# Performance work log

Hardware: AMD Instinct MI355X
Metric: run time of the kernel (lower is better)

Reference implementation:

```python
import jax, jax.numpy as jnp
import numpy as np

N, E, D, H = 100000, 1600000, 128, 2
D2 = D * H  # conv2 output dim = out_dim * heads = 256


def setup_inputs() -> dict:
    key = jax.random.key(0)
    ks = jax.random.split(key, 9)
    x = jax.random.normal(ks[0], (N, D), dtype=jnp.float32)
    edge_index = jax.random.randint(ks[1], (2, E), 0, N, dtype=jnp.int64)
    edge_weight = jax.random.uniform(ks[2], (E,), dtype=jnp.float32)
    s = 1.0 / np.sqrt(D)
    W_rel1 = jax.random.normal(ks[3], (D, D), dtype=jnp.float32) * s
    W_root1 = jax.random.normal(ks[4], (D, D), dtype=jnp.float32) * s
    b1 = jnp.zeros((D,), dtype=jnp.float32)
    W_rel2 = jax.random.normal(ks[5], (D, D2), dtype=jnp.float32) * s
    W_root2 = jax.random.normal(ks[6], (D, D2), dtype=jnp.float32) * s
    b2 = jnp.zeros((D2,), dtype=jnp.float32)
    return {"x": x, "edge_index": edge_index, "edge_weight": edge_weight,
            "W_rel1": W_rel1, "b1": b1, "W_root1": W_root1,
            "W_rel2": W_rel2, "b2": b2, "W_root2": W_root2}


def _graph_conv(x, src, dst, edge_weight, W_rel, b, W_root, n_nodes):
    # message: w_e * x_src ; aggregate: mean over incoming edges at dst
    msgs = x[src] * edge_weight[:, None]                       # [E, D]
    summed = jax.ops.segment_sum(msgs, dst, num_segments=n_nodes)  # [N, D]
    cnt = jax.ops.segment_sum(jnp.ones((src.shape[0],), x.dtype), dst,
                              num_segments=n_nodes)
    mean = summed / jnp.maximum(cnt, 1.0)[:, None]
    # GraphConv: lin_rel(aggr) + lin_root(x); bias only on lin_rel
    return mean @ W_rel + b + x @ W_root


def reference(x, edge_index, edge_weight, W_rel1, b1, W_root1, W_rel2, b2, W_root2):
    src, dst = edge_index[0], edge_index[1]
    n = x.shape[0]
    h = _graph_conv(x, src, dst, edge_weight, W_rel1, b1, W_root1, n)
    out = _graph_conv(h, src, dst, edge_weight, W_rel2, b2, W_root2, n)
    return out
```

## Files before the change

### kernel.cpp

```cpp
#include <hip/hip_runtime.h>
#include <hip/hip_bf16.h>

#define D_IN 128
#define SORT_CHUNK 4096
#define NBUCK 256

typedef __attribute__((ext_vector_type(8))) short bf16x8;
typedef __attribute__((ext_vector_type(8))) unsigned short u16x8;
typedef __attribute__((ext_vector_type(4))) float f32x4;


__global__ __launch_bounds__(256) void scan_block_sums(const int* __restrict__ in,
                                                       int* __restrict__ partial,
                                                       int M) {
    __shared__ int sdata[256];
    int b = blockIdx.x, t = threadIdx.x;
    int base = b * 1024 + t * 4;
    int s = 0;
#pragma unroll
    for (int i = 0; i < 4; ++i) {
        int idx = base + i;
        if (idx < M) s += in[idx];
    }
    sdata[t] = s;
    __syncthreads();
    for (int off = 128; off > 0; off >>= 1) {
        if (t < off) sdata[t] += sdata[t + off];
        __syncthreads();
    }
    if (t == 0) partial[b] = sdata[0];
}

__global__ void scan_partials(int* __restrict__ partial, int nb) {
    if (threadIdx.x == 0 && blockIdx.x == 0) {
        int run = 0;
        for (int i = 0; i < nb; ++i) {
            int t = partial[i];
            partial[i] = run;
            run += t;
        }
    }
}

__global__ __launch_bounds__(256) void scan_final(const int* __restrict__ in,
                                                  const int* __restrict__ partial,
                                                  int* __restrict__ outS,
                                                  int M) {
    __shared__ int sdata[256];
    int b = blockIdx.x, t = threadIdx.x;
    int base = b * 1024 + t * 4;
    int v[4];
    int s = 0;
#pragma unroll
    for (int i = 0; i < 4; ++i) {
        int idx = base + i;
        v[i] = (idx < M) ? in[idx] : 0;
        s += v[i];
    }
    sdata[t] = s;
    __syncthreads();
    for (int o = 1; o < 256; o <<= 1) {
        int tmp = 0;
        if (t >= o) tmp = sdata[t - o];
        __syncthreads();
        sdata[t] += tmp;
        __syncthreads();
    }
    int run = partial[b] + (sdata[t] - s);
#pragma unroll
    for (int i = 0; i < 4; ++i) {
        int idx = base + i;
        if (idx < M) outS[idx] = run;
        run += v[i];
    }
}


__global__ __launch_bounds__(256) void bucket_hist_kernel(const int* __restrict__ dst,
                                                          int* __restrict__ bh,
                                                          long long E, int N, int nbe) {
    __shared__ int cnt[NBUCK];
    cnt[threadIdx.x] = 0;
    __syncthreads();
    long long base = (long long)blockIdx.x * SORT_CHUNK;
    long long end = base + SORT_CHUNK;
    if (end > E) end = E;
    for (long long i = base + threadIdx.x; i < end; i += 256) {
        int b = (int)(((long long)dst[i] << 8) / N);
        atomicAdd(&cnt[b], 1);
    }
    __syncthreads();
    bh[threadIdx.x * nbe + blockIdx.x] = cnt[threadIdx.x];
}

__global__ __launch_bounds__(256) void bucket_scatter_kernel(const int* __restrict__ src,
                                                             const int* __restrict__ dst,
                                                             const float* __restrict__ ew,
                                                             const int* __restrict__ S,
                                                             int2* __restrict__ tmp_edges,
                                                             int* __restrict__ tmp_dst,
                                                             long long E, int N, int nbe) {
    __shared__ int base_lds[NBUCK];
    __shared__ int cnt[NBUCK];
    base_lds[threadIdx.x] = S[threadIdx.x * nbe + blockIdx.x];
    cnt[threadIdx.x] = 0;
    __syncthreads();
    long long b0 = (long long)blockIdx.x * SORT_CHUNK;
    long long e1 = b0 + SORT_CHUNK;
    if (e1 > E) e1 = E;
    for (long long i = b0 + threadIdx.x; i < e1; i += 256) {
        int d = dst[i];
        int b = (int)(((long long)d << 8) / N);
        int p = base_lds[b] + atomicAdd(&cnt[b], 1);
        tmp_edges[p] = make_int2(src[i], __float_as_int(ew[i]));
        tmp_dst[p] = d;
    }
}

__global__ __launch_bounds__(256) void bucket_sort_kernel(const int* __restrict__ S,
                                                          const int2* __restrict__ tmp_edges,
                                                          const int* __restrict__ tmp_dst,
                                                          int2* __restrict__ edges,
                                                          int* __restrict__ hist,
                                                          int* __restrict__ off,
                                                          long long E, int N, int nbe) {
    __shared__ int cnt[512];
    __shared__ int tsum[256];
    __shared__ int pos[512];
    const int b = blockIdx.x, t = threadIdx.x;
    const int lo = (int)(((long long)b * N + 255) >> 8);
    const int hi = (int)(((long long)(b + 1) * N + 255) >> 8);
    const int start = S[b * nbe];
    const int end = (b == NBUCK - 1) ? (int)E : S[(b + 1) * nbe];

    cnt[t] = 0;
    cnt[t + 256] = 0;
    __syncthreads();
    for (int i = start + t; i < end; i += 256)
        atomicAdd(&cnt[tmp_dst[i] - lo], 1);
    __syncthreads();

    int a0 = cnt[2 * t], a1 = cnt[2 * t + 1];
    tsum[t] = a0 + a1;
    __syncthreads();
    for (int o = 1; o < 256; o <<= 1) {
        int v = (t >= o) ? tsum[t - o] : 0;
        __syncthreads();
        tsum[t] += v;
        __syncthreads();
    }
    int excl = tsum[t] - (a0 + a1);
    pos[2 * t]     = start + excl;
    pos[2 * t + 1] = start + excl + a0;

    int d0 = lo + 2 * t, d1 = lo + 2 * t + 1;
    if (d0 < hi) { hist[d0] = a0; off[d0] = start + excl + a0; }
    if (d1 < hi) { hist[d1] = a1; off[d1] = start + excl + a0 + a1; }
    __syncthreads();

    for (int i = start + t; i < end; i += 256) {
        int d = tmp_dst[i] - lo;
        int r = atomicAdd(&pos[d], 1);
        edges[r] = tmp_edges[i];
    }
}


__global__ __launch_bounds__(256) void conv_x_kernel(const float* __restrict__ x,
                                                     __hip_bfloat16* __restrict__ xb,
                                                     long long total4) {
    long long i = (long long)blockIdx.x * 256 + threadIdx.x;
    if (i >= total4) return;
    float4 v = reinterpret_cast<const float4*>(x)[i];
    union { ushort4 u; __hip_bfloat162 h2[2]; } o;
    o.h2[0] = __float22bfloat162_rn(make_float2(v.x, v.y));
    o.h2[1] = __float22bfloat162_rn(make_float2(v.z, v.w));
    reinterpret_cast<ushort4*>(xb)[i] = o.u;
}

template <int DOUT>
__global__ __launch_bounds__(256) void conv_w_kernel(const float* __restrict__ Wrel,
                                                     const float* __restrict__ Wroot,
                                                     __hip_bfloat16* __restrict__ Wt) {
    int idx = blockIdx.x * 256 + threadIdx.x;
    if (idx >= DOUT * 256) return;
    int strip  = idx >> 14;
    int within = idx & 16383;
    int s      = within >> 3;
    int j      = within & 7;
    int kchunk = s >> 6;
    int col    = s & 63;
    int k      = kchunk * 8 + j;
    int jcol   = strip * 64 + col;
    float v = (k < 128) ? Wrel[(size_t)k * DOUT + jcol]
                        : Wroot[(size_t)(k - 128) * DOUT + jcol];
    Wt[idx] = __float2bfloat16(v);
}

__global__ __launch_bounds__(256) void aggregate_kernel(const __hip_bfloat16* __restrict__ featb,
                                                        const int2* __restrict__ edges,
                                                        const int* __restrict__ off,
                                                        const int* __restrict__ hist,
                                                        __hip_bfloat16* __restrict__ aggb,
                                                        int N) {
    int node = blockIdx.x * 4 + (threadIdx.x >> 6);
    if (node >= N) return;
    const int lane = threadIdx.x & 63;
    const int g = lane >> 4;
    const int sub = lane & 15;
    const int cnt = hist[node];
    const int end = off[node];
    const int start = end - cnt;
    const float inv = 1.0f / fmaxf((float)cnt, 1.0f);

    const ushort* fb = (const ushort*)featb;
    float acc[8] = {0.f, 0.f, 0.f, 0.f, 0.f, 0.f, 0.f, 0.f};

    int e = start + g;
    for (; e + 4 < end; e += 8) {
        int2 e0 = edges[e];
        int2 e1 = edges[e + 4];
        float w0 = __int_as_float(e0.y);
        float w1 = __int_as_float(e1.y);
        u16x8 r0 = *reinterpret_cast<const u16x8*>(fb + (size_t)e0.x * 128 + sub * 8);
        u16x8 r1 = *reinterpret_cast<const u16x8*>(fb + (size_t)e1.x * 128 + sub * 8);
#pragma unroll
        for (int j = 0; j < 8; ++j) {
            acc[j] += w0 * __int_as_float((unsigned)r0[j] << 16)
                    + w1 * __int_as_float((unsigned)r1[j] << 16);
        }
    }
    if (e < end) {
        int2 e0 = edges[e];
        float w0 = __int_as_float(e0.y);
        u16x8 r0 = *reinterpret_cast<const u16x8*>(fb + (size_t)e0.x * 128 + sub * 8);
#pragma unroll
        for (int j = 0; j < 8; ++j)
            acc[j] += w0 * __int_as_float((unsigned)r0[j] << 16);
    }

#pragma unroll
    for (int j = 0; j < 8; ++j) {
        acc[j] += __shfl_xor(acc[j], 16, 64);
        acc[j] += __shfl_xor(acc[j], 32, 64);
    }

    if (g == 0) {
        union { u16x8 u; __hip_bfloat162 h2[4]; } o;
#pragma unroll
        for (int j = 0; j < 4; ++j)
            o.h2[j] = __float22bfloat162_rn(make_float2(acc[2 * j] * inv, acc[2 * j + 1] * inv));
        *reinterpret_cast<u16x8*>((ushort*)aggb + (size_t)node * 128 + sub * 8) = o.u;
    }
}

template <int DOUT, bool OUT_BF16>
__global__ __launch_bounds__(256, 2) void gemm_mfma6(const __hip_bfloat16* __restrict__ Arel,
                                                     const __hip_bfloat16* __restrict__ Aroot,
                                                     const __hip_bfloat16* __restrict__ Wt,
                                                     const float* __restrict__ bias,
                                                     void* __restrict__ outp,
                                                     int M) {
    constexpr int NY = DOUT / 64;
    __shared__ __align__(16) unsigned char As[32768];
    __shared__ __align__(16) unsigned char Bs[32768];

    const int nb = gridDim.x;
    const int orig = blockIdx.x;
    const int xcd = orig & 7;
    const int lid = orig >> 3;
    const int q = nb >> 3, r = nb & 7;
    const int wgid = (xcd < r ? xcd * (q + 1) : r * (q + 1) + (xcd - r) * q) + lid;

    const int ty = wgid % NY;
    const int tx = wgid / NY;
    const int tid = threadIdx.x;
    const int lane = tid & 63;
    const int wave = tid >> 6;
    const int lr = lane & 15;
    const int lk = lane >> 4;

    const char* wbase = (const char*)Wt + (size_t)ty * 32768;
#pragma unroll
    for (int i = 0; i < 8; ++i) {
        int s = i * 256 + tid;
        __builtin_amdgcn_global_load_lds(
            (const __attribute__((address_space(1))) unsigned int*)(wbase + (size_t)s * 16),
            (__attribute__((address_space(3))) unsigned int*)(&Bs[s * 16]),
            16, 0, 0);
    }
#pragma unroll
    for (int i = 0; i < 8; ++i) {
        int s = i * 256 + tid;
        int kc = s >> 6;
        int rloc = s & 63;
        int row = tx * 64 + rloc;
        int rc = row < M ? row : M - 1;
        const short* srcp = (i < 4)
            ? (const short*)Arel  + (size_t)rc * 128 + kc * 8
            : (const short*)Aroot + (size_t)rc * 128 + (kc - 16) * 8;
        __builtin_amdgcn_global_load_lds(
            (const __attribute__((address_space(1))) unsigned int*)srcp,
            (__attribute__((address_space(3))) unsigned int*)(&As[s * 16]),
            16, 0, 0);
    }

    const int wr = wave >> 1;
    const int wc = wave & 1;
    const int mloc = wr * 32;
    const int nloc = wc * 32;

    __syncthreads();

    f32x4 zero = {0.f, 0.f, 0.f, 0.f};
    f32x4 acc[2][2] = {{zero, zero}, {zero, zero}};

#pragma unroll
    for (int kk = 0; kk < 8; ++kk) {
        const int chunk = kk * 4 + lk;
        bf16x8 a[2], b[2];
#pragma unroll
        for (int mi = 0; mi < 2; ++mi)
            a[mi] = *reinterpret_cast<const bf16x8*>(&As[(chunk * 64 + mloc + mi * 16 + lr) * 16]);
#pragma unroll
        for (int ni = 0; ni < 2; ++ni)
            b[ni] = *reinterpret_cast<const bf16x8*>(&Bs[(chunk * 64 + nloc + ni * 16 + lr) * 16]);
#pragma unroll
        for (int mi = 0; mi < 2; ++mi)
#pragma unroll
            for (int ni = 0; ni < 2; ++ni)
                acc[mi][ni] = __builtin_amdgcn_mfma_f32_16x16x32_bf16(a[mi], b[ni], acc[mi][ni], 0, 0, 0);
    }

#pragma unroll
    for (int mi = 0; mi < 2; ++mi)
#pragma unroll
        for (int ni = 0; ni < 2; ++ni) {
            int col = ty * 64 + nloc + ni * 16 + lr;
            float bv = bias[col];
#pragma unroll
            for (int rr = 0; rr < 4; ++rr) {
                int row = tx * 64 + mloc + mi * 16 + lk * 4 + rr;
                if (row < M) {
                    float v = acc[mi][ni][rr] + bv;
                    if (OUT_BF16)
                        ((__hip_bfloat16*)outp)[(size_t)row * DOUT + col] = __float2bfloat16(v);
                    else
                        __builtin_nontemporal_store(v, (float*)outp + (size_t)row * DOUT + col);
                }
            }
        }
}


extern "C" void kernel_launch(void* const* d_in, const int* in_sizes, int n_in,
                              void* d_out, int out_size, void* d_ws, size_t ws_size,
                              hipStream_t stream) {
    const float* x      = (const float*)d_in[0];
    const int*   ei     = (const int*)d_in[1];
    const float* ew     = (const float*)d_in[2];
    const float* Wrel1  = (const float*)d_in[3];
    const float* b1     = (const float*)d_in[4];
    const float* Wroot1 = (const float*)d_in[5];
    const float* Wrel2  = (const float*)d_in[6];
    const float* b2     = (const float*)d_in[7];
    const float* Wroot2 = (const float*)d_in[8];
    float* out = (float*)d_out;

    const int N = in_sizes[0] / D_IN;
    const long long E = in_sizes[2];
    const int* src = ei;
    const int* dst = ei + E;

    const int nbe = (int)((E + SORT_CHUNK - 1) / SORT_CHUNK);
    const int M = nbe * NBUCK;
    const int nbM = (M + 1023) / 1024;

    int* hist = (int*)d_ws;
    int* off  = hist + N;
    int* part = off + N;
    int2* edges = (int2*)(part + 128);
    __hip_bfloat16* agg1b = (__hip_bfloat16*)(edges + E);
    __hip_bfloat16* xb    = agg1b + (size_t)N * D_IN;
    __hip_bfloat16* agg2b = xb    + (size_t)N * D_IN;
    __hip_bfloat16* hb    = agg2b + (size_t)N * D_IN;
    __hip_bfloat16* Wt1   = hb    + (size_t)N * D_IN;
    __hip_bfloat16* Wt2   = Wt1   + 128 * 256;

    int* bh      = (int*)agg1b;
    int* S       = bh + M;
    int* tmp_dst = S + M;
    int2* tmp_edges = (int2*)agg2b;

    bucket_hist_kernel<<<nbe, 256, 0, stream>>>(dst, bh, E, N, nbe);
    scan_block_sums<<<nbM, 256, 0, stream>>>(bh, part, M);
    scan_partials<<<1, 64, 0, stream>>>(part, nbM);
    scan_final<<<nbM, 256, 0, stream>>>(bh, part, S, M);
    bucket_scatter_kernel<<<nbe, 256, 0, stream>>>(src, dst, ew, S, tmp_edges, tmp_dst, E, N, nbe);
    bucket_sort_kernel<<<NBUCK, 256, 0, stream>>>(S, tmp_edges, tmp_dst, edges, hist, off, E, N, nbe);

    {
        long long total4 = (long long)N * D_IN / 4;
        conv_x_kernel<<<(int)((total4 + 255) / 256), 256, 0, stream>>>(x, xb, total4);
        conv_w_kernel<128><<<(128 * 256 + 255) / 256, 256, 0, stream>>>(Wrel1, Wroot1, Wt1);
        conv_w_kernel<256><<<(256 * 256 + 255) / 256, 256, 0, stream>>>(Wrel2, Wroot2, Wt2);
    }

    const int ab = (N + 3) / 4;
    const int gx64 = (N + 63) / 64;

    aggregate_kernel<<<ab, 256, 0, stream>>>(xb, edges, off, hist, agg1b, N);
    gemm_mfma6<128, true><<<gx64 * 2, 256, 0, stream>>>(agg1b, xb, Wt1, b1, hb, N);

    aggregate_kernel<<<ab, 256, 0, stream>>>(hb, edges, off, hist, agg2b, N);
    gemm_mfma6<256, false><<<gx64 * 4, 256, 0, stream>>>(agg2b, hb, Wt2, b2, out, N);
}
```

Baseline: 308.7 us.

## Make GEMM persistent over 32-row panels with double-buffered A staging

Replaces the one-tile-per-block GEMM with a persistent kernel. Each block loads its 64-column weight slice into LDS once, then walks a range of 32-row panels. The A panel for the next iteration is prefetched into a second LDS buffer while MFMAs run on the current one. This removes repeated weight loads and launch-tail overhead, and also switches the fp32 output from nontemporal to normal stores. In exchange it uses fewer blocks, adds a barrier per panel and runs fewer MFMAs per wave per step.

```diff
diff --git a/kernel.cpp b/kernel.cpp
--- a/kernel.cpp
+++ b/kernel.cpp
@@ -255,30 +255,35 @@
 }
 
 template <int DOUT, bool OUT_BF16>
-__global__ __launch_bounds__(256, 2) void gemm_mfma6(const __hip_bfloat16* __restrict__ Arel,
+__global__ __launch_bounds__(256, 2) void gemm_mfma7(const __hip_bfloat16* __restrict__ Arel,
                                                      const __hip_bfloat16* __restrict__ Aroot,
                                                      const __hip_bfloat16* __restrict__ Wt,
                                                      const float* __restrict__ bias,
                                                      void* __restrict__ outp,
-                                                     int M) {
-    constexpr int NY = DOUT / 64;
-    __shared__ __align__(16) unsigned char As[32768];
+                                                     int M, int per_strip, int ppb) {
     __shared__ __align__(16) unsigned char Bs[32768];
+    __shared__ __align__(16) unsigned char As[2][16384];
 
     const int nb = gridDim.x;
     const int orig = blockIdx.x;
     const int xcd = orig & 7;
-    const int lid = orig >> 3;
+    const int lid0 = orig >> 3;
     const int q = nb >> 3, r = nb & 7;
-    const int wgid = (xcd < r ? xcd * (q + 1) : r * (q + 1) + (xcd - r) * q) + lid;
-
-    const int ty = wgid % NY;
-    const int tx = wgid / NY;
+    const int wgid = (xcd < r ? xcd * (q + 1) : r * (q + 1) + (xcd - r) * q) + lid0;
+
+    const int ty = wgid / per_strip;
+    const int lid = wgid % per_strip;
+    const int npan = (M + 31) >> 5;
+    const int p0 = lid * ppb;
+    const int pend = min(p0 + ppb, npan);
+
     const int tid = threadIdx.x;
     const int lane = tid & 63;
     const int wave = tid >> 6;
     const int lr = lane & 15;
     const int lk = lane >> 4;
+    const int wr = wave >> 1;
+    const int wc = wave & 1;
 
     const char* wbase = (const char*)Wt + (size_t)ty * 32768;
 #pragma unroll
@@ -289,67 +294,64 @@
             (__attribute__((address_space(3))) unsigned int*)(&Bs[s * 16]),
             16, 0, 0);
     }
-#pragma unroll
-    for (int i = 0; i < 8; ++i) {
-        int s = i * 256 + tid;
-        int kc = s >> 6;
-        int rloc = s & 63;
-        int row = tx * 64 + rloc;
-        int rc = row < M ? row : M - 1;
-        const short* srcp = (i < 4)
-            ? (const short*)Arel  + (size_t)rc * 128 + kc * 8
-            : (const short*)Aroot + (size_t)rc * 128 + (kc - 16) * 8;
-        __builtin_amdgcn_global_load_lds(
-            (const __attribute__((address_space(1))) unsigned int*)srcp,
-            (__attribute__((address_space(3))) unsigned int*)(&As[s * 16]),
-            16, 0, 0);
-    }
-
-    const int wr = wave >> 1;
-    const int wc = wave & 1;
-    const int mloc = wr * 32;
-    const int nloc = wc * 32;
-
+
+    auto stageA = [&](int panel, int buf) {
+#pragma unroll
+        for (int i = 0; i < 4; ++i) {
+            int s = i * 256 + tid;
+            int kc = s >> 5;
+            int rloc = s & 31;
+            int row = panel * 32 + rloc;
+            int rc = row < M ? row : M - 1;
+            const short* srcp = (kc < 16)
+                ? (const short*)Arel  + (size_t)rc * 128 + kc * 8
+                : (const short*)Aroot + (size_t)rc * 128 + (kc - 16) * 8;
+            __builtin_amdgcn_global_load_lds(
+                (const __attribute__((address_space(1))) unsigned int*)srcp,
+                (__attribute__((address_space(3))) unsigned int*)(&As[buf][s * 16]),
+                16, 0, 0);
+        }
+    };
+
+    if (p0 < pend) stageA(p0, 0);
     __syncthreads();
 
     f32x4 zero = {0.f, 0.f, 0.f, 0.f};
-    f32x4 acc[2][2] = {{zero, zero}, {zero, zero}};
-
-#pragma unroll
-    for (int kk = 0; kk < 8; ++kk) {
-        const int chunk = kk * 4 + lk;
-        bf16x8 a[2], b[2];
-#pragma unroll
-        for (int mi = 0; mi < 2; ++mi)
-            a[mi] = *reinterpret_cast<const bf16x8*>(&As[(chunk * 64 + mloc + mi * 16 + lr) * 16]);
-#pragma unroll
-        for (int ni = 0; ni < 2; ++ni)
-            b[ni] = *reinterpret_cast<const bf16x8*>(&Bs[(chunk * 64 + nloc + ni * 16 + lr) * 16]);
-#pragma unroll
-        for (int mi = 0; mi < 2; ++mi)
-#pragma unroll
-            for (int ni = 0; ni < 2; ++ni)
-                acc[mi][ni] = __builtin_amdgcn_mfma_f32_16x16x32_bf16(a[mi], b[ni], acc[mi][ni], 0, 0, 0);
-    }
-
-#pragma unroll
-    for (int mi = 0; mi < 2; ++mi)
+
+    for (int p = p0; p < pend; ++p) {
+        const int cur = (p - p0) & 1;
+        if (p + 1 < pend) stageA(p + 1, cur ^ 1);
+
+        f32x4 acc0 = zero, acc1 = zero;
+#pragma unroll
+        for (int kk = 0; kk < 8; ++kk) {
+            const int chunk = kk * 4 + lk;
+            bf16x8 a  = *reinterpret_cast<const bf16x8*>(&As[cur][(chunk * 32 + wr * 16 + lr) * 16]);
+            bf16x8 b0 = *reinterpret_cast<const bf16x8*>(&Bs[(chunk * 64 + wc * 32 + lr) * 16]);
+            bf16x8 b1 = *reinterpret_cast<const bf16x8*>(&Bs[(chunk * 64 + wc * 32 + 16 + lr) * 16]);
+            acc0 = __builtin_amdgcn_mfma_f32_16x16x32_bf16(a, b0, acc0, 0, 0, 0);
+            acc1 = __builtin_amdgcn_mfma_f32_16x16x32_bf16(a, b1, acc1, 0, 0, 0);
+        }
+
 #pragma unroll
         for (int ni = 0; ni < 2; ++ni) {
-            int col = ty * 64 + nloc + ni * 16 + lr;
+            int col = ty * 64 + wc * 32 + ni * 16 + lr;
             float bv = bias[col];
+            const f32x4& av = ni ? acc1 : acc0;
 #pragma unroll
             for (int rr = 0; rr < 4; ++rr) {
-                int row = tx * 64 + mloc + mi * 16 + lk * 4 + rr;
+                int row = p * 32 + wr * 16 + lk * 4 + rr;
                 if (row < M) {
-                    float v = acc[mi][ni][rr] + bv;
+                    float v = av[rr] + bv;
                     if (OUT_BF16)
                         ((__hip_bfloat16*)outp)[(size_t)row * DOUT + col] = __float2bfloat16(v);
                     else
-                        __builtin_nontemporal_store(v, (float*)outp + (size_t)row * DOUT + col);
+                        ((float*)outp)[(size_t)row * DOUT + col] = v;
                 }
             }
         }
+        __syncthreads();
+    }
 }
 
 
@@ -407,11 +409,19 @@
     }
 
     const int ab = (N + 3) / 4;
-    const int gx64 = (N + 63) / 64;
+    const int npan = (N + 31) >> 5;
 
     aggregate_kernel<<<ab, 256, 0, stream>>>(xb, edges, off, hist, agg1b, N);
-    gemm_mfma6<128, true><<<gx64 * 2, 256, 0, stream>>>(agg1b, xb, Wt1, b1, hb, N);
+    {
+        int per_strip = 256;
+        int ppb = (npan + per_strip - 1) / per_strip;
+        gemm_mfma7<128, true><<<2 * per_strip, 256, 0, stream>>>(agg1b, xb, Wt1, b1, hb, N, per_strip, ppb);
+    }
 
     aggregate_kernel<<<ab, 256, 0, stream>>>(hb, edges, off, hist, agg2b, N);
-    gemm_mfma6<256, false><<<gx64 * 4, 256, 0, stream>>>(agg2b, hb, Wt2, b2, out, N);
-}
+    {
+        int per_strip = 128;
+        int ppb = (npan + per_strip - 1) / per_strip;
+        gemm_mfma7<256, false><<<4 * per_strip, 256, 0, stream>>>(agg2b, hb, Wt2, b2, out, N, per_strip, ppb);
+    }
+}
```

Measured after the change: 318.7 us. 1.03x slower.

## Overlap root GEMM with neighbor aggregation in one interleaved kernel

Applied to the files above, without the earlier changes.

Splits each GraphConv GEMM into a root part (x @ W_root + b) and a rel part (mean @ W_rel). The root part now runs in the same launch as the edge aggregation: the grid interleaves one GEMM block with every RATIO aggregation blocks, so compute-bound MFMA work overlaps the memory-bound gather. A separate K=128 rel GEMM then adds its result onto the stored root partial. The cost is an extra bf16 write and read of the intermediate, extra bf16 rounding of the layer-2 partial, and plain rather than nontemporal stores for the final output.

```diff
diff --git a/kernel.cpp b/kernel.cpp
--- a/kernel.cpp
+++ b/kernel.cpp
@@ -179,31 +179,28 @@
 }
 
 template <int DOUT>
-__global__ __launch_bounds__(256) void conv_w_kernel(const float* __restrict__ Wrel,
-                                                     const float* __restrict__ Wroot,
-                                                     __hip_bfloat16* __restrict__ Wt) {
+__global__ __launch_bounds__(256) void conv_wt_kernel(const float* __restrict__ W,
+                                                      __hip_bfloat16* __restrict__ Wt) {
     int idx = blockIdx.x * 256 + threadIdx.x;
-    if (idx >= DOUT * 256) return;
-    int strip  = idx >> 14;
-    int within = idx & 16383;
+    if (idx >= DOUT * 128) return;
+    int strip  = idx >> 13;
+    int within = idx & 8191;
     int s      = within >> 3;
     int j      = within & 7;
-    int kchunk = s >> 6;
+    int kc     = s >> 6;
     int col    = s & 63;
-    int k      = kchunk * 8 + j;
+    int k      = kc * 8 + j;
     int jcol   = strip * 64 + col;
-    float v = (k < 128) ? Wrel[(size_t)k * DOUT + jcol]
-                        : Wroot[(size_t)(k - 128) * DOUT + jcol];
-    Wt[idx] = __float2bfloat16(v);
-}
-
-__global__ __launch_bounds__(256) void aggregate_kernel(const __hip_bfloat16* __restrict__ featb,
-                                                        const int2* __restrict__ edges,
-                                                        const int* __restrict__ off,
-                                                        const int* __restrict__ hist,
-                                                        __hip_bfloat16* __restrict__ aggb,
-                                                        int N) {
-    int node = blockIdx.x * 4 + (threadIdx.x >> 6);
+    Wt[idx] = __float2bfloat16(W[(size_t)k * DOUT + jcol]);
+}
+
+__device__ __forceinline__ void agg_body(const __hip_bfloat16* __restrict__ featb,
+                                         const int2* __restrict__ edges,
+                                         const int* __restrict__ off,
+                                         const int* __restrict__ hist,
+                                         __hip_bfloat16* __restrict__ aggb,
+                                         int N, int abid) {
+    int node = abid * 4 + (threadIdx.x >> 6);
     if (node >= N) return;
     const int lane = threadIdx.x & 63;
     const int g = lane >> 4;
@@ -254,35 +251,30 @@
     }
 }
 
-template <int DOUT, bool OUT_BF16>
-__global__ __launch_bounds__(256, 2) void gemm_mfma6(const __hip_bfloat16* __restrict__ Arel,
-                                                     const __hip_bfloat16* __restrict__ Aroot,
-                                                     const __hip_bfloat16* __restrict__ Wt,
-                                                     const float* __restrict__ bias,
-                                                     void* __restrict__ outp,
-                                                     int M) {
-    constexpr int NY = DOUT / 64;
-    __shared__ __align__(16) unsigned char As[32768];
-    __shared__ __align__(16) unsigned char Bs[32768];
-
-    const int nb = gridDim.x;
-    const int orig = blockIdx.x;
-    const int xcd = orig & 7;
-    const int lid = orig >> 3;
-    const int q = nb >> 3, r = nb & 7;
-    const int wgid = (xcd < r ? xcd * (q + 1) : r * (q + 1) + (xcd - r) * q) + lid;
-
-    const int ty = wgid % NY;
-    const int tx = wgid / NY;
+template <int DOUT, bool ADD, bool OUT_BF16>
+__device__ __forceinline__ void gemm128_body(const __hip_bfloat16* __restrict__ A,
+                                             const __hip_bfloat16* __restrict__ Wt,
+                                             const float* __restrict__ bias,
+                                             const __hip_bfloat16* __restrict__ addsrc,
+                                             void* __restrict__ outp,
+                                             int M, int bid, unsigned char* lds) {
+    constexpr int STRIPS = DOUT / 64;
+    unsigned char* As = lds;
+    unsigned char* Bs = lds + 16384;
+
+    const int ty = bid % STRIPS;
+    const int tx = bid / STRIPS;
     const int tid = threadIdx.x;
     const int lane = tid & 63;
     const int wave = tid >> 6;
     const int lr = lane & 15;
     const int lk = lane >> 4;
-
-    const char* wbase = (const char*)Wt + (size_t)ty * 32768;
-#pragma unroll
-    for (int i = 0; i < 8; ++i) {
+    const int wr = wave >> 1;
+    const int wc = wave & 1;
+
+    const char* wbase = (const char*)Wt + (size_t)ty * 16384;
+#pragma unroll
+    for (int i = 0; i < 4; ++i) {
         int s = i * 256 + tid;
         __builtin_amdgcn_global_load_lds(
             (const __attribute__((address_space(1))) unsigned int*)(wbase + (size_t)s * 16),
@@ -290,41 +282,33 @@
             16, 0, 0);
     }
 #pragma unroll
-    for (int i = 0; i < 8; ++i) {
+    for (int i = 0; i < 4; ++i) {
         int s = i * 256 + tid;
         int kc = s >> 6;
         int rloc = s & 63;
         int row = tx * 64 + rloc;
         int rc = row < M ? row : M - 1;
-        const short* srcp = (i < 4)
-            ? (const short*)Arel  + (size_t)rc * 128 + kc * 8
-            : (const short*)Aroot + (size_t)rc * 128 + (kc - 16) * 8;
+        const short* srcp = (const short*)A + (size_t)rc * 128 + kc * 8;
         __builtin_amdgcn_global_load_lds(
             (const __attribute__((address_space(1))) unsigned int*)srcp,
             (__attribute__((address_space(3))) unsigned int*)(&As[s * 16]),
             16, 0, 0);
     }
-
-    const int wr = wave >> 1;
-    const int wc = wave & 1;
-    const int mloc = wr * 32;
-    const int nloc = wc * 32;
-
     __syncthreads();
 
     f32x4 zero = {0.f, 0.f, 0.f, 0.f};
     f32x4 acc[2][2] = {{zero, zero}, {zero, zero}};
 
 #pragma unroll
-    for (int kk = 0; kk < 8; ++kk) {
+    for (int kk = 0; kk < 4; ++kk) {
         const int chunk = kk * 4 + lk;
         bf16x8 a[2], b[2];
 #pragma unroll
         for (int mi = 0; mi < 2; ++mi)
-            a[mi] = *reinterpret_cast<const bf16x8*>(&As[(chunk * 64 + mloc + mi * 16 + lr) * 16]);
+            a[mi] = *reinterpret_cast<const bf16x8*>(&As[(chunk * 64 + wr * 32 + mi * 16 + lr) * 16]);
 #pragma unroll
         for (int ni = 0; ni < 2; ++ni)
-            b[ni] = *reinterpret_cast<const bf16x8*>(&Bs[(chunk * 64 + nloc + ni * 16 + lr) * 16]);
+            b[ni] = *reinterpret_cast<const bf16x8*>(&Bs[(chunk * 64 + wc * 32 + ni * 16 + lr) * 16]);
 #pragma unroll
         for (int mi = 0; mi < 2; ++mi)
 #pragma unroll
@@ -336,20 +320,56 @@
     for (int mi = 0; mi < 2; ++mi)
 #pragma unroll
         for (int ni = 0; ni < 2; ++ni) {
-            int col = ty * 64 + nloc + ni * 16 + lr;
-            float bv = bias[col];
+            int col = ty * 64 + wc * 32 + ni * 16 + lr;
+            float bv = ADD ? 0.f : bias[col];
 #pragma unroll
             for (int rr = 0; rr < 4; ++rr) {
-                int row = tx * 64 + mloc + mi * 16 + lk * 4 + rr;
+                int row = tx * 64 + wr * 32 + mi * 16 + lk * 4 + rr;
                 if (row < M) {
                     float v = acc[mi][ni][rr] + bv;
+                    if (ADD)
+                        v += __bfloat162float(addsrc[(size_t)row * DOUT + col]);
                     if (OUT_BF16)
                         ((__hip_bfloat16*)outp)[(size_t)row * DOUT + col] = __float2bfloat16(v);
                     else
-                        __builtin_nontemporal_store(v, (float*)outp + (size_t)row * DOUT + col);
+                        ((float*)outp)[(size_t)row * DOUT + col] = v;
                 }
             }
         }
+}
+
+template <int DOUT, int RATIO>
+__global__ __launch_bounds__(256, 2) void fused_root_agg(const __hip_bfloat16* __restrict__ featb,
+                                                         const int2* __restrict__ edges,
+                                                         const int* __restrict__ off,
+                                                         const int* __restrict__ hist,
+                                                         __hip_bfloat16* __restrict__ aggb,
+                                                         const __hip_bfloat16* __restrict__ Wt,
+                                                         const float* __restrict__ bias,
+                                                         __hip_bfloat16* __restrict__ outg,
+                                                         int N, int G_g, int G_a) {
+    __shared__ __align__(16) unsigned char lds[32768];
+    const int bid = blockIdx.x;
+    const int g = bid / (RATIO + 1);
+    const int r = bid % (RATIO + 1);
+    if (r == RATIO) {
+        if (g < G_g)
+            gemm128_body<DOUT, false, true>(featb, Wt, bias, nullptr, outg, N, g, lds);
+    } else {
+        int a = g * RATIO + r;
+        if (a < G_a)
+            agg_body(featb, edges, off, hist, aggb, N, a);
+    }
+}
+
+template <int DOUT, bool OUT_BF16>
+__global__ __launch_bounds__(256, 2) void gemm_rel_kernel(const __hip_bfloat16* __restrict__ A,
+                                                          const __hip_bfloat16* __restrict__ Wt,
+                                                          const __hip_bfloat16* __restrict__ addsrc,
+                                                          void* __restrict__ outp,
+                                                          int M) {
+    __shared__ __align__(16) unsigned char lds[32768];
+    gemm128_body<DOUT, true, OUT_BF16>(A, Wt, nullptr, addsrc, outp, M, blockIdx.x, lds);
 }
 
 
@@ -384,8 +404,12 @@
     __hip_bfloat16* xb    = agg1b + (size_t)N * D_IN;
     __hip_bfloat16* agg2b = xb    + (size_t)N * D_IN;
     __hip_bfloat16* hb    = agg2b + (size_t)N * D_IN;
-    __hip_bfloat16* Wt1   = hb    + (size_t)N * D_IN;
-    __hip_bfloat16* Wt2   = Wt1   + 128 * 256;
+    __hip_bfloat16* Wl1t  = hb    + (size_t)N * D_IN;
+    __hip_bfloat16* Wr1t  = Wl1t  + 128 * 128;
+    __hip_bfloat16* Wl2t  = Wr1t  + 128 * 128;
+    __hip_bfloat16* Wr2t  = Wl2t  + 256 * 128;
+
+    __hip_bfloat16* tmp2 = agg1b;
 
     int* bh      = (int*)agg1b;
     int* S       = bh + M;
@@ -402,16 +426,28 @@
     {
         long long total4 = (long long)N * D_IN / 4;
         conv_x_kernel<<<(int)((total4 + 255) / 256), 256, 0, stream>>>(x, xb, total4);
-        conv_w_kernel<128><<<(128 * 256 + 255) / 256, 256, 0, stream>>>(Wrel1, Wroot1, Wt1);
-        conv_w_kernel<256><<<(256 * 256 + 255) / 256, 256, 0, stream>>>(Wrel2, Wroot2, Wt2);
-    }
-
-    const int ab = (N + 3) / 4;
-    const int gx64 = (N + 63) / 64;
-
-    aggregate_kernel<<<ab, 256, 0, stream>>>(xb, edges, off, hist, agg1b, N);
-    gemm_mfma6<128, true><<<gx64 * 2, 256, 0, stream>>>(agg1b, xb, Wt1, b1, hb, N);
-
-    aggregate_kernel<<<ab, 256, 0, stream>>>(hb, edges, off, hist, agg2b, N);
-    gemm_mfma6<256, false><<<gx64 * 4, 256, 0, stream>>>(agg2b, hb, Wt2, b2, out, N);
-}
+        conv_wt_kernel<128><<<(128 * 128 + 255) / 256, 256, 0, stream>>>(Wrel1, Wl1t);
+        conv_wt_kernel<128><<<(128 * 128 + 255) / 256, 256, 0, stream>>>(Wroot1, Wr1t);
+        conv_wt_kernel<256><<<(256 * 128 + 255) / 256, 256, 0, stream>>>(Wrel2, Wl2t);
+        conv_wt_kernel<256><<<(256 * 128 + 255) / 256, 256, 0, stream>>>(Wroot2, Wr2t);
+    }
+
+    const int G_a = (N + 3) / 4;
+    const int npan64 = (N + 63) / 64;
+
+    {
+        const int G_g = npan64 * 2;
+        int groups = max(G_g, (G_a + 7) / 8);
+        fused_root_agg<128, 8><<<groups * 9, 256, 0, stream>>>(
+            xb, edges, off, hist, agg1b, Wr1t, b1, hb, N, G_g, G_a);
+        gemm_rel_kernel<128, true><<<G_g, 256, 0, stream>>>(agg1b, Wl1t, hb, hb, N);
+    }
+
+    {
+        const int G_g = npan64 * 4;
+        int groups = max(G_g, (G_a + 3) / 4);
+        fused_root_agg<256, 4><<<groups * 5, 256, 0, stream>>>(
+            hb, edges, off, hist, agg2b, Wr2t, b2, tmp2, N, G_g, G_a);
+        gemm_rel_kernel<256, false><<<G_g, 256, 0, stream>>>(agg2b, Wl2t, tmp2, out, N);
+    }
+}
```

Measured after the change: 445.2 us. 1.44x slower.
